# Kernel tuning notes

Measured on AMD Instinct MI355X. Metric: run time of the kernel, lower is better.

The kernel has to match this reference:

```python
import jax, jax.numpy as jnp
import numpy as np

TEMP = 0.5
ALPHA = 1.0
BETA = 5.5
GAMMA = 5.0
N, D, C, M = 400, 512, 1000, 16000


def _normalize(x, axis=-1, eps=1e-12):
    return x / jnp.maximum(jnp.linalg.norm(x, axis=axis, keepdims=True), eps)


def _scale(x, target):
    # min-max scale x into the value range of target (global scalars)
    y = (x - x.min()) / (x.max() - x.min())
    y = y * (target.max() - target.min())
    y = y + target.min()
    return y


def setup_inputs() -> dict:
    key = jax.random.key(0)
    k1, k2, k3, k4 = jax.random.split(key, 4)
    image_features = jax.random.normal(k1, (N, D), dtype=jnp.float32)
    text_embeds = jax.random.normal(k2, (C, D), dtype=jnp.float32)
    support_feats = _normalize(jax.random.normal(k3, (D, M), dtype=jnp.float32), axis=0)
    support_labels = jax.random.randint(k4, (M,), 0, C)
    return {
        "image_features": image_features,
        "text_embeds": text_embeds,
        "support_feats": support_feats,
        "support_labels": support_labels,
    }


def reference(image_features, text_embeds, support_feats, support_labels):
    # one-hot support targets [M, C]
    support_targets = jax.nn.one_hot(support_labels, C, dtype=jnp.float32)

    # L2-normalize features (forward() normalizes both text and image features)
    text_features = _normalize(text_embeds, axis=-1).T          # [D, C]
    img = _normalize(image_features, axis=-1)                   # [N, D]

    # class distributions via temperature softmax
    train_logits = (support_feats.T @ text_features) / TEMP     # [M, C]
    test_logits = (img @ text_features) / TEMP                  # [N, C]
    train_log_dist = jax.nn.log_softmax(train_logits, axis=-1)  # log q  [M, C]
    test_log_dist = jax.nn.log_softmax(test_logits, axis=-1)    # log p  [N, C]
    test_dist = jnp.exp(test_log_dist)                          # p      [N, C]

    # KL(p_i || q_j) = sum_c p_ic log p_ic - sum_c p_ic log q_jc  -> one GEMM
    entropy_term = jnp.sum(test_dist * test_log_dist, axis=-1, keepdims=True)  # [N, 1]
    kl_divs = entropy_term - test_dist @ train_log_dist.T                      # [N, M]

    clip_logits = 100.0 * (img @ text_features)                 # [N, C]
    new_knowledge = img @ support_feats                         # [N, M]

    neg_affs = _scale(kl_divs, new_knowledge)                   # [N, M]
    affinities = -neg_affs
    kl_logits = affinities @ support_targets                    # [N, C]
    cache_logits = jnp.exp(-(BETA - BETA * new_knowledge)) @ support_targets  # [N, C]

    tipx_logits = clip_logits + kl_logits * GAMMA + cache_logits * ALPHA
    return tipx_logits
```

## Files before the change

### kernel.cpp

```cpp
#include <hip/hip_runtime.h>
#include <math.h>

#define TEMP_F   0.5f
#define ALPHA_F  1.0f
#define BETA_F   5.5f
#define GAMMA_F  5.0f
#define N_IMG    400
#define D_DIM    512
#define C_CLS    1000
#define C_PAD    1024
#define M_SUP    16000

typedef __attribute__((ext_vector_type(8))) short short8;
typedef __attribute__((ext_vector_type(4))) short short4v;
typedef __attribute__((ext_vector_type(4))) float f32x4;

__device__ __forceinline__ short f2bf(float f) {
    unsigned u = __float_as_uint(f);
    unsigned r = (u + 0x7fffu + ((u >> 16) & 1u)) >> 16;
    return (short)r;
}
__device__ __forceinline__ float bf2f(short s) {
    return __uint_as_float(((unsigned)(unsigned short)s) << 16);
}
__device__ __forceinline__ unsigned encf(float f) {
    unsigned u = __float_as_uint(f);
    return (u & 0x80000000u) ? ~u : (u | 0x80000000u);
}
__device__ __forceinline__ float decf(unsigned u) {
    return (u & 0x80000000u) ? __uint_as_float(u & 0x7FFFFFFFu) : __uint_as_float(~u);
}

__device__ __forceinline__ float block_reduce_sum(float v) {
    __shared__ float red[4];
    #pragma unroll
    for (int o = 32; o > 0; o >>= 1) v += __shfl_down(v, o, 64);
    int w = threadIdx.x >> 6, l = threadIdx.x & 63;
    __syncthreads();
    if (l == 0) red[w] = v;
    __syncthreads();
    float r = red[0];
    int nw = blockDim.x >> 6;
    for (int i = 1; i < nw; ++i) r += red[i];
    return r;
}

__device__ __forceinline__ void gload_lds16(const void* g, void* l) {
    __builtin_amdgcn_global_load_lds(
        (const __attribute__((address_space(1))) unsigned int*)g,
        (__attribute__((address_space(3))) unsigned int*)l, 16, 0, 0);
}

__global__ void init_mm_k(unsigned* mm) {
    mm[0] = encf(INFINITY);
    mm[1] = encf(-INFINITY);
    mm[2] = encf(INFINITY);
    mm[3] = encf(-INFINITY);
}

__global__ void normalize_rows_k(const float* __restrict__ src, short* __restrict__ dst) {
    int row = blockIdx.x;
    const float* s = src + (long)row * D_DIM;
    short* d = dst + (long)row * D_DIM;
    float ss = 0.f;
    for (int c = threadIdx.x; c < D_DIM; c += blockDim.x) { float v = s[c]; ss += v * v; }
    float tot = block_reduce_sum(ss);
    float inv = 1.0f / fmaxf(sqrtf(tot), 1e-12f);
    for (int c = threadIdx.x; c < D_DIM; c += blockDim.x) d[c] = f2bf(s[c] * inv);
}

__global__ void transpose_bf16_k(const float* __restrict__ S, short* __restrict__ Sb) {
    __shared__ float tile[64][65];
    int m0 = blockIdx.x * 64, d0 = blockIdx.y * 64;
    int ml = (threadIdx.x & 15) * 4;
    int dl = threadIdx.x >> 4;
    #pragma unroll
    for (int r = 0; r < 64; r += 16) {
        f32x4 v = *(const f32x4*)(S + (long)(d0 + dl + r) * M_SUP + m0 + ml);
        tile[dl + r][ml + 0] = v[0];
        tile[dl + r][ml + 1] = v[1];
        tile[dl + r][ml + 2] = v[2];
        tile[dl + r][ml + 3] = v[3];
    }
    __syncthreads();
    int mw = threadIdx.x >> 4;
    int dc = (threadIdx.x & 15) * 4;
    #pragma unroll
    for (int r = 0; r < 64; r += 16) {
        short4v o;
        #pragma unroll
        for (int k = 0; k < 4; ++k) o[k] = f2bf(tile[dc + k][mw + r]);
        *(short4v*)(Sb + (long)(m0 + mw + r) * D_DIM + d0 + dc) = o;
    }
}

template<int EPI, int SWZ>
__global__ __launch_bounds__(256) void mfma_gemm(
    const short* __restrict__ A, const short* __restrict__ B, void* __restrict__ Cm,
    int I, int Jclamp, int Jout, int K, long lda, long ldb, long ldc, float alpha,
    const float* __restrict__ ent, const float* __restrict__ lse,
    unsigned* __restrict__ mm, float* __restrict__ out2)
{
    __shared__ short As[3][128 * 32];
    __shared__ short Bs[3][128 * 32];
    const int tid = threadIdx.x;
    const int wave = tid >> 6;
    const int lane = tid & 63;

    int i0, j0;
    if (SWZ == 1) {
        int lin = blockIdx.x;
        int xcd = lin & 7;
        int idx = lin >> 3;
        i0 = (idx & 3) * 128;
        j0 = (xcd * 16 + (idx >> 2)) * 128;
    } else {
        i0 = blockIdx.y * 128;
        j0 = blockIdx.x * 128;
    }

    const int srow = wave * 16 + (lane >> 2);
    const int skk  = (lane & 3) * 8;

    const int wm = (wave & 1) * 64;
    const int wn = (wave >> 1) * 64;
    const int fr = lane & 15;
    const int fq = lane >> 4;

    f32x4 acc[4][4] = {};

    auto stage = [&](int buf, int k0) {
        #pragma unroll
        for (int q = 0; q < 2; ++q) {
            int gi = i0 + q * 64 + srow; if (gi > I - 1) gi = I - 1;
            gload_lds16(A + (long)gi * lda + k0 + skk, As[buf] + q * 2048 + wave * 512);
        }
        #pragma unroll
        for (int q = 0; q < 2; ++q) {
            int gj = j0 + q * 64 + srow; if (gj > Jclamp - 1) gj = Jclamp - 1;
            gload_lds16(B + (long)gj * ldb + k0 + skk, Bs[buf] + q * 2048 + wave * 512);
        }
    };

    const int nt = K >> 5;
    stage(0, 0);
    if (nt > 1) stage(1, 32);
    if (nt > 2) stage(2, 64);

    for (int t = 0; t < nt; ++t) {
        const int b = t % 3;

        if (t + 2 < nt)      asm volatile("s_waitcnt vmcnt(8)" ::: "memory");
        else if (t + 1 < nt) asm volatile("s_waitcnt vmcnt(4)" ::: "memory");
        else                 asm volatile("s_waitcnt vmcnt(0)" ::: "memory");
        __builtin_amdgcn_s_barrier();
        __builtin_amdgcn_sched_barrier(0);

        short8 af[4], bfr[4];
        #pragma unroll
        for (int mi = 0; mi < 4; ++mi)
            af[mi] = *(const short8*)(As[b] + (wm + mi * 16 + fr) * 32 + fq * 8);
        #pragma unroll
        for (int ni = 0; ni < 4; ++ni)
            bfr[ni] = *(const short8*)(Bs[b] + (wn + ni * 16 + fr) * 32 + fq * 8);

        asm volatile("s_waitcnt lgkmcnt(0)" ::: "memory");
        __builtin_amdgcn_sched_barrier(0);
        __builtin_amdgcn_s_barrier();

        if (t + 3 < nt) stage(b, (t + 3) << 5);

        __builtin_amdgcn_s_setprio(1);
        #pragma unroll
        for (int mi = 0; mi < 4; ++mi)
            #pragma unroll
            for (int ni = 0; ni < 4; ++ni)
                acc[mi][ni] = __builtin_amdgcn_mfma_f32_16x16x32_bf16(
                    af[mi], bfr[ni], acc[mi][ni], 0, 0, 0);
        __builtin_amdgcn_s_setprio(0);
    }

    float lmin = INFINITY, lmax = -INFINITY;

    #pragma unroll
    for (int mi = 0; mi < 4; ++mi) {
        #pragma unroll
        for (int ni = 0; ni < 4; ++ni) {
            int gj = j0 + wn + ni * 16 + fr;
            float lsev = 0.f;
            if (EPI == 2) lsev = lse[gj < Jout ? gj : (Jout - 1)];
            #pragma unroll
            for (int t = 0; t < 4; ++t) {
                int gi = i0 + wm + mi * 16 + fq * 4 + t;
                float v = alpha * acc[mi][ni][t];
                if (EPI == 2) {
                    int gic = gi < I ? gi : (I - 1);
                    v = ent[gic] - v + lsev;
                }
                if (EPI == 2 || EPI == 3) { lmin = fminf(lmin, v); lmax = fmaxf(lmax, v); }
                if (gi < I && gj < Jout) {
                    if (EPI == 1) ((short*)Cm)[(long)gi * ldc + gj] = f2bf(v);
                    else          ((float*)Cm)[(long)gi * ldc + gj] = v;
                }
                if (EPI == 4 && gi < I && gj < C_CLS)
                    out2[(long)gi * C_CLS + gj] = 100.f * v;
            }
        }
    }

    if (EPI == 2 || EPI == 3) {
        #pragma unroll
        for (int o = 32; o > 0; o >>= 1) {
            lmin = fminf(lmin, __shfl_down(lmin, o, 64));
            lmax = fmaxf(lmax, __shfl_down(lmax, o, 64));
        }
        __shared__ float rmin[4], rmax[4];
        if (lane == 0) { rmin[wave] = lmin; rmax[wave] = lmax; }
        __syncthreads();
        if (tid == 0) {
            float bmin = fminf(fminf(rmin[0], rmin[1]), fminf(rmin[2], rmin[3]));
            float bmax = fmaxf(fmaxf(rmax[0], rmax[1]), fmaxf(rmax[2], rmax[3]));
            const int base = (EPI == 2) ? 0 : 2;
            atomicMin(&mm[base + 0], encf(bmin));
            atomicMax(&mm[base + 1], encf(bmax));
        }
    }
}

__global__ void row_lse_k(const short* __restrict__ t, float* __restrict__ lse) {
    int row = blockIdx.x * 4 + (threadIdx.x >> 6);
    int lane = threadIdx.x & 63;
    const short* r = t + (long)row * C_PAD;
    short8 v0 = *(const short8*)(r + lane * 8);
    short8 v1 = *(const short8*)(r + 512 + lane * 8);
    bool act1 = lane < 61;
    float f0[8], f1[8];
    float mx = -INFINITY;
    #pragma unroll
    for (int j = 0; j < 8; ++j) { f0[j] = bf2f(v0[j]); mx = fmaxf(mx, f0[j]); }
    if (act1) {
        #pragma unroll
        for (int j = 0; j < 8; ++j) { f1[j] = bf2f(v1[j]); mx = fmaxf(mx, f1[j]); }
    }
    #pragma unroll
    for (int o = 32; o > 0; o >>= 1) mx = fmaxf(mx, __shfl_xor(mx, o, 64));
    float se = 0.f;
    #pragma unroll
    for (int j = 0; j < 8; ++j) se += __expf(f0[j] - mx);
    if (act1) {
        #pragma unroll
        for (int j = 0; j < 8; ++j) se += __expf(f1[j] - mx);
    }
    #pragma unroll
    for (int o = 32; o > 0; o >>= 1) se += __shfl_xor(se, o, 64);
    if (lane == 0) lse[row] = mx + __logf(se);
}

__global__ void test_softmax_k(const float* __restrict__ dot, short* __restrict__ p,
                               float* __restrict__ ent) {
    int n = blockIdx.x * 4 + (threadIdx.x >> 6);
    int lane = threadIdx.x & 63;
    const float* dr = dot + (long)n * C_PAD;
    short* pr = p + (long)n * C_PAD;
    f32x4 v[4];
    #pragma unroll
    for (int pp = 0; pp < 4; ++pp)
        v[pp] = *(const f32x4*)(dr + pp * 256 + lane * 4);
    float mx = -INFINITY;
    #pragma unroll
    for (int pp = 0; pp < 4; ++pp) {
        bool valid = (pp < 3) || (lane < 58);
        if (valid)
            #pragma unroll
            for (int j = 0; j < 4; ++j) mx = fmaxf(mx, 2.f * v[pp][j]);
    }
    #pragma unroll
    for (int o = 32; o > 0; o >>= 1) mx = fmaxf(mx, __shfl_xor(mx, o, 64));
    float se = 0.f;
    #pragma unroll
    for (int pp = 0; pp < 4; ++pp) {
        bool valid = (pp < 3) || (lane < 58);
        if (valid)
            #pragma unroll
            for (int j = 0; j < 4; ++j) se += __expf(2.f * v[pp][j] - mx);
    }
    #pragma unroll
    for (int o = 32; o > 0; o >>= 1) se += __shfl_xor(se, o, 64);
    float logsum = mx + __logf(se);
    float e = 0.f;
    #pragma unroll
    for (int pp = 0; pp < 4; ++pp) {
        bool valid = (pp < 3) || (lane < 58);
        short4v o4;
        #pragma unroll
        for (int j = 0; j < 4; ++j) {
            if (valid) {
                float lp = 2.f * v[pp][j] - logsum;
                float pv = __expf(lp);
                o4[j] = f2bf(pv);
                e += pv * lp;
            } else {
                o4[j] = 0;
            }
        }
        *(short4v*)(pr + pp * 256 + lane * 4) = o4;
    }
    #pragma unroll
    for (int o = 32; o > 0; o >>= 1) e += __shfl_xor(e, o, 64);
    if (lane == 0) ent[n] = e;
}

__global__ __launch_bounds__(256) void final_partial_k(
    const float* __restrict__ kl, const float* __restrict__ nk,
    const int* __restrict__ labels, const unsigned* __restrict__ mm,
    float* __restrict__ out)
{
    int n = blockIdx.x;
    int q = blockIdx.y;
    __shared__ float bins[C_CLS];
    for (int c = threadIdx.x; c < C_CLS; c += 256) bins[c] = 0.f;
    __syncthreads();
    float klmin = decf(mm[0]), klmax = decf(mm[1]);
    float nkmin = decf(mm[2]), nkmax = decf(mm[3]);
    float ratio = (nkmax - nkmin) / (klmax - klmin);
    const int m0 = q * (M_SUP / 4);
    const float4* kl4 = (const float4*)(kl + (long)n * M_SUP + m0);
    const float4* nk4 = (const float4*)(nk + (long)n * M_SUP + m0);
    const int4*  lb4 = (const int4*)(labels + m0);
    const int nv = M_SUP / 4 / 4;
    for (int v = threadIdx.x; v < nv; v += 256) {
        float4 kv = kl4[v];
        float4 vv = nk4[v];
        int4   lv = lb4[v];
        float y, contrib;
        y = (kv.x - klmin) * ratio + nkmin;
        contrib = -GAMMA_F * y + ALPHA_F * __expf(BETA_F * (vv.x - 1.0f));
        atomicAdd(&bins[lv.x], contrib);
        y = (kv.y - klmin) * ratio + nkmin;
        contrib = -GAMMA_F * y + ALPHA_F * __expf(BETA_F * (vv.y - 1.0f));
        atomicAdd(&bins[lv.y], contrib);
        y = (kv.z - klmin) * ratio + nkmin;
        contrib = -GAMMA_F * y + ALPHA_F * __expf(BETA_F * (vv.z - 1.0f));
        atomicAdd(&bins[lv.z], contrib);
        y = (kv.w - klmin) * ratio + nkmin;
        contrib = -GAMMA_F * y + ALPHA_F * __expf(BETA_F * (vv.w - 1.0f));
        atomicAdd(&bins[lv.w], contrib);
    }
    __syncthreads();
    for (int c = threadIdx.x; c < C_CLS; c += 256)
        atomicAdd(&out[(long)n * C_CLS + c], bins[c]);
}

extern "C" void kernel_launch(void* const* d_in, const int* in_sizes, int n_in,
                              void* d_out, int out_size, void* d_ws, size_t ws_size,
                              hipStream_t stream) {
    const float* image_features = (const float*)d_in[0];
    const float* text_embeds    = (const float*)d_in[1];
    const float* support_feats  = (const float*)d_in[2];
    const int*   support_labels = (const int*)d_in[3];
    float* out = (float*)d_out;

    char* base = (char*)d_ws;
    size_t off = 0;
    auto alloc = [&](size_t bytes) {
        void* p = base + off;
        off = (off + bytes + 255) & ~(size_t)255;
        return p;
    };
    short* Tnb  = (short*)alloc(sizeof(short) * C_CLS * D_DIM);
    short* imgb = (short*)alloc(sizeof(short) * N_IMG * D_DIM);
    short* Sb   = (short*)alloc(sizeof(short) * M_SUP * D_DIM);
    short* tb   = (short*)alloc(sizeof(short) * M_SUP * C_PAD);
    short* pb   = (short*)alloc(sizeof(short) * N_IMG * C_PAD);
    float* dot  = (float*)alloc(sizeof(float) * N_IMG * C_PAD);
    float* lse  = (float*)alloc(sizeof(float) * M_SUP);
    float* ent  = (float*)alloc(sizeof(float) * N_IMG);
    float* kl   = (float*)alloc(sizeof(float) * N_IMG * M_SUP);
    float* nk   = (float*)alloc(sizeof(float) * N_IMG * M_SUP);
    unsigned* mm = (unsigned*)alloc(256);

    init_mm_k<<<1, 1, 0, stream>>>(mm);
    normalize_rows_k<<<C_CLS, 256, 0, stream>>>(text_embeds, Tnb);
    normalize_rows_k<<<N_IMG, 256, 0, stream>>>(image_features, imgb);
    transpose_bf16_k<<<dim3(M_SUP / 64, D_DIM / 64), 256, 0, stream>>>(support_feats, Sb);

    mfma_gemm<1, 0><<<dim3(8, 125), 256, 0, stream>>>(
        Sb, Tnb, tb, M_SUP, C_CLS, C_PAD, D_DIM, D_DIM, D_DIM, C_PAD, 2.0f,
        nullptr, nullptr, nullptr, nullptr);

    row_lse_k<<<M_SUP / 4, 256, 0, stream>>>(tb, lse);

    mfma_gemm<4, 0><<<dim3(8, 4), 256, 0, stream>>>(
        imgb, Tnb, dot, N_IMG, C_CLS, C_PAD, D_DIM, D_DIM, D_DIM, C_PAD, 1.0f,
        nullptr, nullptr, nullptr, out);

    test_softmax_k<<<N_IMG / 4, 256, 0, stream>>>(dot, pb, ent);

    mfma_gemm<2, 1><<<512, 256, 0, stream>>>(
        pb, tb, kl, N_IMG, M_SUP, M_SUP, C_PAD, C_PAD, C_PAD, M_SUP, 1.0f,
        ent, lse, mm, nullptr);

    mfma_gemm<3, 1><<<512, 256, 0, stream>>>(
        imgb, Sb, nk, N_IMG, M_SUP, M_SUP, D_DIM, D_DIM, D_DIM, M_SUP, 1.0f,
        nullptr, nullptr, mm, nullptr);

    final_partial_k<<<dim3(N_IMG, 4), 256, 0, stream>>>(kl, nk, support_labels, mm, out);
}
```

Before: 243.9 us.

## Merge independent kernels into combined launches to cut launch count and tails

Merges init, row normalization and transpose into one prep kernel. The three GEMMs that depend only on the prep outputs (train logits, new_knowledge, test dot) now run as block ranges of a single kernel, and the row-LSE and test softmax share one launch. The KL GEMM keeps its own launch. The aim is fewer launches (10 down to 5) and independent work filling the GPU together rather than small grids leaving it idle. The cost is larger kernels whose register use and occupancy follow the heaviest branch.

```diff
diff --git a/kernel.cpp b/kernel.cpp
--- a/kernel.cpp
+++ b/kernel.cpp
@@ -51,73 +51,17 @@
         (__attribute__((address_space(3))) unsigned int*)l, 16, 0, 0);
 }
 
-__global__ void init_mm_k(unsigned* mm) {
-    mm[0] = encf(INFINITY);
-    mm[1] = encf(-INFINITY);
-    mm[2] = encf(INFINITY);
-    mm[3] = encf(-INFINITY);
-}
-
-__global__ void normalize_rows_k(const float* __restrict__ src, short* __restrict__ dst) {
-    int row = blockIdx.x;
-    const float* s = src + (long)row * D_DIM;
-    short* d = dst + (long)row * D_DIM;
-    float ss = 0.f;
-    for (int c = threadIdx.x; c < D_DIM; c += blockDim.x) { float v = s[c]; ss += v * v; }
-    float tot = block_reduce_sum(ss);
-    float inv = 1.0f / fmaxf(sqrtf(tot), 1e-12f);
-    for (int c = threadIdx.x; c < D_DIM; c += blockDim.x) d[c] = f2bf(s[c] * inv);
-}
-
-__global__ void transpose_bf16_k(const float* __restrict__ S, short* __restrict__ Sb) {
-    __shared__ float tile[64][65];
-    int m0 = blockIdx.x * 64, d0 = blockIdx.y * 64;
-    int ml = (threadIdx.x & 15) * 4;
-    int dl = threadIdx.x >> 4;
-    #pragma unroll
-    for (int r = 0; r < 64; r += 16) {
-        f32x4 v = *(const f32x4*)(S + (long)(d0 + dl + r) * M_SUP + m0 + ml);
-        tile[dl + r][ml + 0] = v[0];
-        tile[dl + r][ml + 1] = v[1];
-        tile[dl + r][ml + 2] = v[2];
-        tile[dl + r][ml + 3] = v[3];
-    }
-    __syncthreads();
-    int mw = threadIdx.x >> 4;
-    int dc = (threadIdx.x & 15) * 4;
-    #pragma unroll
-    for (int r = 0; r < 64; r += 16) {
-        short4v o;
-        #pragma unroll
-        for (int k = 0; k < 4; ++k) o[k] = f2bf(tile[dc + k][mw + r]);
-        *(short4v*)(Sb + (long)(m0 + mw + r) * D_DIM + d0 + dc) = o;
-    }
-}
-
-template<int EPI, int SWZ>
-__global__ __launch_bounds__(256) void mfma_gemm(
+template<int EPI>
+__device__ __forceinline__ void gemm_body(
     const short* __restrict__ A, const short* __restrict__ B, void* __restrict__ Cm,
     int I, int Jclamp, int Jout, int K, long lda, long ldb, long ldc, float alpha,
     const float* __restrict__ ent, const float* __restrict__ lse,
-    unsigned* __restrict__ mm, float* __restrict__ out2)
-{
-    __shared__ short As[3][128 * 32];
-    __shared__ short Bs[3][128 * 32];
+    unsigned* __restrict__ mm, float* __restrict__ out2,
+    int i0, int j0, short (*As)[4096], short (*Bs)[4096])
+{
     const int tid = threadIdx.x;
     const int wave = tid >> 6;
     const int lane = tid & 63;
-
-    int i0, j0;
-    if (SWZ == 1) {
-        int lin = blockIdx.x;
-        int xcd = lin & 7;
-        int idx = lin >> 3;
-        i0 = (idx & 3) * 128;
-        j0 = (xcd * 16 + (idx >> 2)) * 128;
-    } else {
-        i0 = blockIdx.y * 128;
-        j0 = blockIdx.x * 128;
-    }
 
     const int srow = wave * 16 + (lane >> 2);
     const int skk  = (lane & 3) * 8;
@@ -227,87 +171,186 @@
     }
 }
 
-__global__ void row_lse_k(const short* __restrict__ t, float* __restrict__ lse) {
-    int row = blockIdx.x * 4 + (threadIdx.x >> 6);
-    int lane = threadIdx.x & 63;
-    const short* r = t + (long)row * C_PAD;
-    short8 v0 = *(const short8*)(r + lane * 8);
-    short8 v1 = *(const short8*)(r + 512 + lane * 8);
-    bool act1 = lane < 61;
-    float f0[8], f1[8];
-    float mx = -INFINITY;
-    #pragma unroll
-    for (int j = 0; j < 8; ++j) { f0[j] = bf2f(v0[j]); mx = fmaxf(mx, f0[j]); }
-    if (act1) {
-        #pragma unroll
-        for (int j = 0; j < 8; ++j) { f1[j] = bf2f(v1[j]); mx = fmaxf(mx, f1[j]); }
-    }
-    #pragma unroll
-    for (int o = 32; o > 0; o >>= 1) mx = fmaxf(mx, __shfl_xor(mx, o, 64));
-    float se = 0.f;
-    #pragma unroll
-    for (int j = 0; j < 8; ++j) se += __expf(f0[j] - mx);
-    if (act1) {
-        #pragma unroll
-        for (int j = 0; j < 8; ++j) se += __expf(f1[j] - mx);
-    }
-    #pragma unroll
-    for (int o = 32; o > 0; o >>= 1) se += __shfl_xor(se, o, 64);
-    if (lane == 0) lse[row] = mx + __logf(se);
-}
-
-__global__ void test_softmax_k(const float* __restrict__ dot, short* __restrict__ p,
-                               float* __restrict__ ent) {
-    int n = blockIdx.x * 4 + (threadIdx.x >> 6);
-    int lane = threadIdx.x & 63;
-    const float* dr = dot + (long)n * C_PAD;
-    short* pr = p + (long)n * C_PAD;
-    f32x4 v[4];
-    #pragma unroll
-    for (int pp = 0; pp < 4; ++pp)
-        v[pp] = *(const f32x4*)(dr + pp * 256 + lane * 4);
-    float mx = -INFINITY;
-    #pragma unroll
-    for (int pp = 0; pp < 4; ++pp) {
-        bool valid = (pp < 3) || (lane < 58);
-        if (valid)
-            #pragma unroll
-            for (int j = 0; j < 4; ++j) mx = fmaxf(mx, 2.f * v[pp][j]);
-    }
-    #pragma unroll
-    for (int o = 32; o > 0; o >>= 1) mx = fmaxf(mx, __shfl_xor(mx, o, 64));
-    float se = 0.f;
-    #pragma unroll
-    for (int pp = 0; pp < 4; ++pp) {
-        bool valid = (pp < 3) || (lane < 58);
-        if (valid)
-            #pragma unroll
-            for (int j = 0; j < 4; ++j) se += __expf(2.f * v[pp][j] - mx);
-    }
-    #pragma unroll
-    for (int o = 32; o > 0; o >>= 1) se += __shfl_xor(se, o, 64);
-    float logsum = mx + __logf(se);
-    float e = 0.f;
-    #pragma unroll
-    for (int pp = 0; pp < 4; ++pp) {
-        bool valid = (pp < 3) || (lane < 58);
-        short4v o4;
-        #pragma unroll
-        for (int j = 0; j < 4; ++j) {
-            if (valid) {
-                float lp = 2.f * v[pp][j] - logsum;
-                float pv = __expf(lp);
-                o4[j] = f2bf(pv);
-                e += pv * lp;
-            } else {
-                o4[j] = 0;
+
+__global__ __launch_bounds__(256) void prep_k(
+    const float* __restrict__ text_embeds, const float* __restrict__ image_features,
+    const float* __restrict__ S,
+    short* __restrict__ Tnb, short* __restrict__ imgb, short* __restrict__ Sb,
+    unsigned* __restrict__ mm)
+{
+    const int b = blockIdx.x;
+    if (b == 0 && threadIdx.x < 4)
+        mm[threadIdx.x] = (threadIdx.x & 1) ? encf(-INFINITY) : encf(INFINITY);
+
+    if (b < 1400) {
+        const float* s;
+        short* d;
+        if (b < 1000) { s = text_embeds + (long)b * D_DIM;            d = Tnb  + (long)b * D_DIM; }
+        else          { s = image_features + (long)(b - 1000) * D_DIM; d = imgb + (long)(b - 1000) * D_DIM; }
+        float ss = 0.f;
+        for (int c = threadIdx.x; c < D_DIM; c += 256) { float v = s[c]; ss += v * v; }
+        float tot = block_reduce_sum(ss);
+        float inv = 1.0f / fmaxf(sqrtf(tot), 1e-12f);
+        for (int c = threadIdx.x; c < D_DIM; c += 256) d[c] = f2bf(s[c] * inv);
+    } else {
+        __shared__ float tile[64][65];
+        int l = b - 1400;
+        int m0 = (l % 250) * 64, d0 = (l / 250) * 64;
+        int ml = (threadIdx.x & 15) * 4;
+        int dl = threadIdx.x >> 4;
+        #pragma unroll
+        for (int r = 0; r < 64; r += 16) {
+            f32x4 v = *(const f32x4*)(S + (long)(d0 + dl + r) * M_SUP + m0 + ml);
+            tile[dl + r][ml + 0] = v[0];
+            tile[dl + r][ml + 1] = v[1];
+            tile[dl + r][ml + 2] = v[2];
+            tile[dl + r][ml + 3] = v[3];
+        }
+        __syncthreads();
+        int mw = threadIdx.x >> 4;
+        int dc = (threadIdx.x & 15) * 4;
+        #pragma unroll
+        for (int r = 0; r < 64; r += 16) {
+            short4v o;
+            #pragma unroll
+            for (int k = 0; k < 4; ++k) o[k] = f2bf(tile[dc + k][mw + r]);
+            *(short4v*)(Sb + (long)(m0 + mw + r) * D_DIM + d0 + dc) = o;
+        }
+    }
+}
+
+__global__ __launch_bounds__(256) void mega_gemm_k(
+    const short* __restrict__ Sb, const short* __restrict__ Tnb,
+    const short* __restrict__ imgb,
+    short* __restrict__ tb, float* __restrict__ nk, float* __restrict__ dot,
+    unsigned* __restrict__ mm, float* __restrict__ out)
+{
+    __shared__ short As[3][4096];
+    __shared__ short Bs[3][4096];
+    const int lin = blockIdx.x;
+
+    if (lin < 1000) {
+        int gt = (lin & 7) * 125 + (lin >> 3);
+        int i0 = (gt >> 3) * 128;
+        int j0 = (gt & 7) * 128;
+        gemm_body<1>(Sb, Tnb, tb, M_SUP, C_CLS, C_PAD, D_DIM, D_DIM, D_DIM, C_PAD,
+                     2.0f, nullptr, nullptr, nullptr, nullptr, i0, j0, As, Bs);
+    } else if (lin < 1512) {
+        int l = lin - 1000;
+        int xcd = l & 7;
+        int idx = l >> 3;
+        int i0 = (idx & 3) * 128;
+        int j0 = (xcd * 16 + (idx >> 2)) * 128;
+        gemm_body<3>(imgb, Sb, nk, N_IMG, M_SUP, M_SUP, D_DIM, D_DIM, D_DIM, M_SUP,
+                     1.0f, nullptr, nullptr, mm, nullptr, i0, j0, As, Bs);
+    } else {
+        int l = lin - 1512;
+        int i0 = (l >> 3) * 128;
+        int j0 = (l & 7) * 128;
+        gemm_body<4>(imgb, Tnb, dot, N_IMG, C_CLS, C_PAD, D_DIM, D_DIM, D_DIM, C_PAD,
+                     1.0f, nullptr, nullptr, nullptr, out, i0, j0, As, Bs);
+    }
+}
+
+__global__ void lse_softmax_k(
+    const short* __restrict__ tb, float* __restrict__ lse,
+    const float* __restrict__ dot, short* __restrict__ pb, float* __restrict__ ent)
+{
+    const int b = blockIdx.x;
+    const int lane = threadIdx.x & 63;
+    if (b < 4000) {
+        int row = b * 4 + (threadIdx.x >> 6);
+        const short* r = tb + (long)row * C_PAD;
+        short8 v0 = *(const short8*)(r + lane * 8);
+        short8 v1 = *(const short8*)(r + 512 + lane * 8);
+        bool act1 = lane < 61;
+        float f0[8], f1[8];
+        float mx = -INFINITY;
+        #pragma unroll
+        for (int j = 0; j < 8; ++j) { f0[j] = bf2f(v0[j]); mx = fmaxf(mx, f0[j]); }
+        if (act1) {
+            #pragma unroll
+            for (int j = 0; j < 8; ++j) { f1[j] = bf2f(v1[j]); mx = fmaxf(mx, f1[j]); }
+        }
+        #pragma unroll
+        for (int o = 32; o > 0; o >>= 1) mx = fmaxf(mx, __shfl_xor(mx, o, 64));
+        float se = 0.f;
+        #pragma unroll
+        for (int j = 0; j < 8; ++j) se += __expf(f0[j] - mx);
+        if (act1) {
+            #pragma unroll
+            for (int j = 0; j < 8; ++j) se += __expf(f1[j] - mx);
+        }
+        #pragma unroll
+        for (int o = 32; o > 0; o >>= 1) se += __shfl_xor(se, o, 64);
+        if (lane == 0) lse[row] = mx + __logf(se);
+    } else {
+        int n = (b - 4000) * 4 + (threadIdx.x >> 6);
+        const float* dr = dot + (long)n * C_PAD;
+        short* pr = pb + (long)n * C_PAD;
+        f32x4 v[4];
+        #pragma unroll
+        for (int pp = 0; pp < 4; ++pp)
+            v[pp] = *(const f32x4*)(dr + pp * 256 + lane * 4);
+        float mx = -INFINITY;
+        #pragma unroll
+        for (int pp = 0; pp < 4; ++pp) {
+            bool valid = (pp < 3) || (lane < 58);
+            if (valid)
+                #pragma unroll
+                for (int j = 0; j < 4; ++j) mx = fmaxf(mx, 2.f * v[pp][j]);
+        }
+        #pragma unroll
+        for (int o = 32; o > 0; o >>= 1) mx = fmaxf(mx, __shfl_xor(mx, o, 64));
+        float se = 0.f;
+        #pragma unroll
+        for (int pp = 0; pp < 4; ++pp) {
+            bool valid = (pp < 3) || (lane < 58);
+            if (valid)
+                #pragma unroll
+                for (int j = 0; j < 4; ++j) se += __expf(2.f * v[pp][j] - mx);
+        }
+        #pragma unroll
+        for (int o = 32; o > 0; o >>= 1) se += __shfl_xor(se, o, 64);
+        float logsum = mx + __logf(se);
+        float e = 0.f;
+        #pragma unroll
+        for (int pp = 0; pp < 4; ++pp) {
+            bool valid = (pp < 3) || (lane < 58);
+            short4v o4;
+            #pragma unroll
+            for (int j = 0; j < 4; ++j) {
+                if (valid) {
+                    float lp = 2.f * v[pp][j] - logsum;
+                    float pv = __expf(lp);
+                    o4[j] = f2bf(pv);
+                    e += pv * lp;
+                } else {
+                    o4[j] = 0;
+                }
             }
-        }
-        *(short4v*)(pr + pp * 256 + lane * 4) = o4;
-    }
-    #pragma unroll
-    for (int o = 32; o > 0; o >>= 1) e += __shfl_xor(e, o, 64);
-    if (lane == 0) ent[n] = e;
+            *(short4v*)(pr + pp * 256 + lane * 4) = o4;
+        }
+        #pragma unroll
+        for (int o = 32; o > 0; o >>= 1) e += __shfl_xor(e, o, 64);
+        if (lane == 0) ent[n] = e;
+    }
+}
+
+__global__ __launch_bounds__(256) void gemm2_k(
+    const short* __restrict__ pb, const short* __restrict__ tb, float* __restrict__ kl,
+    const float* __restrict__ ent, const float* __restrict__ lse,
+    unsigned* __restrict__ mm)
+{
+    __shared__ short As[3][4096];
+    __shared__ short Bs[3][4096];
+    int lin = blockIdx.x;
+    int xcd = lin & 7;
+    int idx = lin >> 3;
+    int i0 = (idx & 3) * 128;
+    int j0 = (xcd * 16 + (idx >> 2)) * 128;
+    gemm_body<2>(pb, tb, kl, N_IMG, M_SUP, M_SUP, C_PAD, C_PAD, C_PAD, M_SUP,
+                 1.0f, ent, lse, mm, nullptr, i0, j0, As, Bs);
 }
 
 __global__ __launch_bounds__(256) void final_partial_k(
@@ -379,30 +422,14 @@
     float* nk   = (float*)alloc(sizeof(float) * N_IMG * M_SUP);
     unsigned* mm = (unsigned*)alloc(256);
 
-    init_mm_k<<<1, 1, 0, stream>>>(mm);
-    normalize_rows_k<<<C_CLS, 256, 0, stream>>>(text_embeds, Tnb);
-    normalize_rows_k<<<N_IMG, 256, 0, stream>>>(image_features, imgb);
-    transpose_bf16_k<<<dim3(M_SUP / 64, D_DIM / 64), 256, 0, stream>>>(support_feats, Sb);
-
-    mfma_gemm<1, 0><<<dim3(8, 125), 256, 0, stream>>>(
-        Sb, Tnb, tb, M_SUP, C_CLS, C_PAD, D_DIM, D_DIM, D_DIM, C_PAD, 2.0f,
-        nullptr, nullptr, nullptr, nullptr);
-
-    row_lse_k<<<M_SUP / 4, 256, 0, stream>>>(tb, lse);
-
-    mfma_gemm<4, 0><<<dim3(8, 4), 256, 0, stream>>>(
-        imgb, Tnb, dot, N_IMG, C_CLS, C_PAD, D_DIM, D_DIM, D_DIM, C_PAD, 1.0f,
-        nullptr, nullptr, nullptr, out);
-
-    test_softmax_k<<<N_IMG / 4, 256, 0, stream>>>(dot, pb, ent);
-
-    mfma_gemm<2, 1><<<512, 256, 0, stream>>>(
-        pb, tb, kl, N_IMG, M_SUP, M_SUP, C_PAD, C_PAD, C_PAD, M_SUP, 1.0f,
-        ent, lse, mm, nullptr);
-
-    mfma_gemm<3, 1><<<512, 256, 0, stream>>>(
-        imgb, Sb, nk, N_IMG, M_SUP, M_SUP, D_DIM, D_DIM, D_DIM, M_SUP, 1.0f,
-        nullptr, nullptr, mm, nullptr);
+    prep_k<<<3400, 256, 0, stream>>>(
+        text_embeds, image_features, support_feats, Tnb, imgb, Sb, mm);
+
+    mega_gemm_k<<<1544, 256, 0, stream>>>(Sb, Tnb, imgb, tb, nk, dot, mm, out);
+
+    lse_softmax_k<<<4100, 256, 0, stream>>>(tb, lse, dot, pb, ent);
+
+    gemm2_k<<<512, 256, 0, stream>>>(pb, tb, kl, ent, lse, mm);
 
     final_partial_k<<<dim3(N_IMG, 4), 256, 0, stream>>>(kl, nk, support_labels, mm, out);
 }
```

Result: faster. 211.4 us (median of 2 runs) (-13.3%).
